# Performance work log

Hardware: AMD Instinct MI355X
Metric: run time of the kernel (lower is better)

## Reference

```python
import jax, jax.numpy as jnp
import numpy as np
import math

B, S, HID = 2, 2048, 2048
NH, HD = 16, HID // 16          # num_heads, head_dim
RING = 4
CH = S // RING                  # chunk size per ring rank
SEG_LEN = 2048                  # segment_lengths[0]
DIL = 2                         # dilation_rates[0]


def setup_inputs() -> dict:
    key = jax.random.key(0)
    k1, k2, k3 = jax.random.split(key, 3)
    x = jax.random.normal(k1, (B, S, HID), dtype=jnp.float32)
    # Linear weights stored input-major so y = x @ W (same math as torch x @ W.T)
    W_qkv = jax.random.normal(k2, (HID, 3 * HID), dtype=jnp.float32) * 0.02
    W_out = jax.random.normal(k3, (HID, HID), dtype=jnp.float32) * 0.02
    return {"x": x, "W_qkv": W_qkv, "W_out": W_out}


def _dilated_mask():
    # mask[i, j] = (segment(i) == segment(j)) and (|i - j| % DIL == 0)
    pos = jnp.arange(S)
    seg = pos // SEG_LEN
    same_seg = seg[:, None] == seg[None, :]
    dil_ok = (jnp.abs(pos[:, None] - pos[None, :]) % DIL) == 0
    return same_seg & dil_ok  # [S, S] bool


def reference(x, W_qkv, W_out):
    qkv = (x @ W_qkv).reshape(B, S, 3, NH, HD)
    q, k, v = jnp.moveaxis(qkv, 2, 0)          # each [B, S, NH, HD]
    q = jnp.transpose(q, (0, 2, 1, 3))          # [B, NH, S, HD]
    k = jnp.transpose(k, (0, 2, 1, 3))
    v = jnp.transpose(v, (0, 2, 1, 3))

    scores = jnp.einsum('bhqd,bhkd->bhqk', q, k) / math.sqrt(HD)  # [B,NH,S,S]
    if DIL > 1:
        scores = jnp.where(_dilated_mask()[None, None], scores, -jnp.inf)

    # Reshape into (q-chunk, kv-chunk) blocks to reproduce the per-chunk
    # (non-rescaled) softmax of the ring loop: each kv chunk subtracts its OWN
    # max, exps, and the un-rescaled numerators/denominators are summed.
    s = scores.reshape(B, NH, RING, CH, RING, CH)        # [B,H,Rq,Cq,Rk,Ck]
    m = jnp.max(s, axis=-1, keepdims=True)               # per-kv-chunk row max
    e = jnp.exp(s - m)                                   # -inf -> 0
    v_ch = v.reshape(B, NH, RING, CH, HD)                # [B,H,Rk,Ck,HD]
    num = jnp.einsum('bhqcrk,bhrkd->bhqcd', e, v_ch)     # [B,H,Rq,Cq,HD]
    den = jnp.sum(e, axis=(-2, -1))[..., None]           # [B,H,Rq,Cq,1]
    out = num / (den + 1e-8)

    out = out.reshape(B, NH, S, HD)
    out = jnp.transpose(out, (0, 2, 1, 3)).reshape(B, S, HID)
    return out @ W_out
```

## Files before the change

kernel.cpp:

```cpp
#include <hip/hip_runtime.h>
#include <stdint.h>

typedef float  f32x4  __attribute__((ext_vector_type(4)));
typedef __bf16 bf16x8 __attribute__((ext_vector_type(8)));

#define AS1 __attribute__((address_space(1)))
#define AS3 __attribute__((address_space(3)))


__global__ void k_cvt_x(const float* __restrict__ x, __bf16* __restrict__ y) {
  const int i = blockIdx.x * 256 + threadIdx.x;
  const float4 v = reinterpret_cast<const float4*>(x)[i];
  union { __bf16 b[4]; uint64_t u; } o;
  o.b[0] = (__bf16)v.x; o.b[1] = (__bf16)v.y; o.b[2] = (__bf16)v.z; o.b[3] = (__bf16)v.w;
  reinterpret_cast<uint64_t*>(y)[i] = o.u;
}

__global__ void k_cvt_wt(const float* __restrict__ w, __bf16* __restrict__ wt,
                         const int K, const int N) {
  __shared__ float tile[64][65];
  const int k0 = blockIdx.x * 64, n0 = blockIdx.y * 64;
  const int t = threadIdx.x;
  #pragma unroll
  for (int i = 0; i < 16; ++i) {
    const int idx = t + 256 * i;
    const int r = idx >> 6, c = idx & 63;
    tile[r][c] = w[(size_t)(k0 + r) * N + n0 + c];
  }
  __syncthreads();
  #pragma unroll
  for (int i = 0; i < 16; ++i) {
    const int idx = t + 256 * i;
    const int r = idx >> 6, c = idx & 63;
    wt[(size_t)(n0 + r) * K + k0 + c] = (__bf16)tile[c][r];
  }
}

template<int EPI>
__global__ __launch_bounds__(256, 2) void k_gemm_bt(
    const __bf16* __restrict__ A, const __bf16* __restrict__ Bt,
    __bf16* __restrict__ Oq, __bf16* __restrict__ Ok, __bf16* __restrict__ Ov,
    float* __restrict__ Of, const int M, const int N, const int K) {
  __shared__ __bf16 As[128 * 32];
  __shared__ __bf16 Bs[128 * 32];
  const int tid = threadIdx.x;
  const int w = tid >> 6, l = tid & 63, g = l >> 4, l15 = l & 15;
  const int wr = w >> 1, wc = w & 1;
  const int m0 = blockIdx.y * 128, n0 = blockIdx.x * 128;
  const int srow = l >> 2, scol = (l & 3) * 8;

  f32x4 acc[4][4] = {};

  for (int kt = 0; kt < K; kt += 32) {
    __syncthreads();
    #pragma unroll
    for (int i = 0; i < 2; ++i) {
      const int ch = w * 2 + i;
      const int row = ch * 16 + srow;
      __builtin_amdgcn_global_load_lds(
          (const AS1 uint32_t*)(A + (size_t)(m0 + row) * K + kt + scol),
          (AS3 uint32_t*)(As + ch * 512), 16, 0, 0);
      __builtin_amdgcn_global_load_lds(
          (const AS1 uint32_t*)(Bt + (size_t)(n0 + row) * K + kt + scol),
          (AS3 uint32_t*)(Bs + ch * 512), 16, 0, 0);
    }
    __syncthreads();

    bf16x8 af[4], bfr[4];
    #pragma unroll
    for (int mi = 0; mi < 4; ++mi)
      af[mi] = *reinterpret_cast<const bf16x8*>(As + (wr * 64 + mi * 16 + l15) * 32 + 8 * g);
    #pragma unroll
    for (int ni = 0; ni < 4; ++ni)
      bfr[ni] = *reinterpret_cast<const bf16x8*>(Bs + (wc * 64 + ni * 16 + l15) * 32 + 8 * g);
    #pragma unroll
    for (int mi = 0; mi < 4; ++mi)
      #pragma unroll
      for (int ni = 0; ni < 4; ++ni)
        acc[mi][ni] = __builtin_amdgcn_mfma_f32_16x16x32_bf16(af[mi], bfr[ni], acc[mi][ni], 0, 0, 0);
  }

  if constexpr (EPI == 1) {
    const int t = n0 >> 11;
    const int h = (n0 & 2047) >> 7;
    const int bb = m0 >> 11;
    #pragma unroll
    for (int mi = 0; mi < 4; ++mi) {
      #pragma unroll
      for (int r = 0; r < 4; ++r) {
        const int m = m0 + wr * 64 + mi * 16 + 4 * g + r;
        const int s = m & 2047;
        const int sp = s & 1, s2 = s >> 1;
        const size_t base = ((((size_t)bb * 16 + h) * 2 + sp) << 17);
        #pragma unroll
        for (int ni = 0; ni < 4; ++ni) {
          const int d = wc * 64 + ni * 16 + l15;
          const __bf16 v = (__bf16)acc[mi][ni][r];
          if (t == 0)      Oq[base + (size_t)s2 * 128 + d] = v;
          else if (t == 1) Ok[base + (size_t)s2 * 128 + d] = v;
          else             Ov[base + (size_t)d * 1024 + s2] = v;
        }
      }
    }
  } else {
    #pragma unroll
    for (int mi = 0; mi < 4; ++mi)
      #pragma unroll
      for (int ni = 0; ni < 4; ++ni)
        #pragma unroll
        for (int r = 0; r < 4; ++r) {
          const int m = m0 + wr * 64 + mi * 16 + 4 * g + r;
          const int n = n0 + wc * 64 + ni * 16 + l15;
          Of[(size_t)m * N + n] = acc[mi][ni][r];
        }
  }
}

__global__ __launch_bounds__(256, 2) void k_attn(
    const __bf16* __restrict__ Qp, const __bf16* __restrict__ Kp,
    const __bf16* __restrict__ Vt, __bf16* __restrict__ attn) {
  __shared__ __bf16 Ks[64 * 128];
  __shared__ __bf16 Vs[128 * 64];
  __shared__ __bf16 E[4][16][136];

  const int bx = blockIdx.x;
  const int wid = (bx & 7) * 128 + (bx >> 3);
  const int qt = wid & 15, p = (wid >> 4) & 1, h = (wid >> 5) & 15, b = wid >> 9;
  const int tid = threadIdx.x;
  const int w = tid >> 6, l = tid & 63, g = l >> 4, l15 = l & 15;
  const size_t base = ((((size_t)b * 16 + h) * 2 + p) << 17);
  const __bf16* Qb = Qp + base;
  const __bf16* Kb = Kp + base;
  const __bf16* Vb = Vt + base;
  const int q0 = qt * 64 + w * 16;
  const float SC = 1.4426950408889634f / 11.313708498984761f;

  bf16x8 qf[4];
  #pragma unroll
  for (int ks = 0; ks < 4; ++ks)
    qf[ks] = *reinterpret_cast<const bf16x8*>(Qb + (size_t)(q0 + l15) * 128 + ks * 32 + 8 * g);

  f32x4 num[8] = {};
  float den[4] = {0.f, 0.f, 0.f, 0.f};

  const int krow_in = l >> 4;
  const int vrow_in = l >> 3;
  const int vsrc_e = (((l & 7) * 16) ^ (vrow_in << 4)) >> 1;

  for (int c = 0; c < 4; ++c) {
    f32x4 s[16] = {};
    #pragma unroll
    for (int st = 0; st < 4; ++st) {
      __syncthreads();
      #pragma unroll
      for (int i = 0; i < 4; ++i) {
        const int ch = w * 4 + i;
        const int row = ch * 4 + krow_in;
        const int cb = (l15 * 16) ^ ((row & 7) << 4);
        const __bf16* src = Kb + (size_t)(c * 256 + st * 64 + row) * 128 + (cb >> 1);
        __builtin_amdgcn_global_load_lds((const AS1 uint32_t*)src,
                                         (AS3 uint32_t*)(Ks + ch * 512), 16, 0, 0);
      }
      __syncthreads();
      #pragma unroll
      for (int ks = 0; ks < 4; ++ks) {
        #pragma unroll
        for (int nf2 = 0; nf2 < 4; ++nf2) {
          const int r = nf2 * 16 + l15;
          const int cb = (ks * 64 + g * 16) ^ ((r & 7) << 4);
          const bf16x8 kf = *reinterpret_cast<const bf16x8*>(Ks + r * 128 + (cb >> 1));
          s[st * 4 + nf2] = __builtin_amdgcn_mfma_f32_16x16x32_bf16(qf[ks], kf, s[st * 4 + nf2], 0, 0, 0);
        }
      }
    }
    float mv[4];
    #pragma unroll
    for (int r = 0; r < 4; ++r) {
      float m0v = s[0][r];
      #pragma unroll
      for (int nf = 1; nf < 16; ++nf) m0v = fmaxf(m0v, s[nf][r]);
      m0v = fmaxf(m0v, __shfl_xor(m0v, 1));
      m0v = fmaxf(m0v, __shfl_xor(m0v, 2));
      m0v = fmaxf(m0v, __shfl_xor(m0v, 4));
      m0v = fmaxf(m0v, __shfl_xor(m0v, 8));
      mv[r] = m0v;
    }
    #pragma unroll
    for (int r = 0; r < 4; ++r) {
      float ds = 0.f;
      #pragma unroll
      for (int nf = 0; nf < 16; ++nf) {
        const float e = exp2f((s[nf][r] - mv[r]) * SC);
        s[nf][r] = e;
        ds += e;
      }
      den[r] += ds;
    }
    #pragma unroll
    for (int h2 = 0; h2 < 2; ++h2) {
      #pragma unroll
      for (int nf = 0; nf < 8; ++nf)
        #pragma unroll
        for (int r = 0; r < 4; ++r)
          E[w][4 * g + r][nf * 16 + l15] = (__bf16)s[h2 * 8 + nf][r];
      #pragma unroll
      for (int sv = 0; sv < 2; ++sv) {
        const int kv0 = c * 256 + h2 * 128 + sv * 64;
        __syncthreads();
        #pragma unroll
        for (int i = 0; i < 4; ++i) {
          const int ch = w * 4 + i;
          const int row = ch * 8 + vrow_in;
          const __bf16* src = Vb + (size_t)row * 1024 + kv0 + vsrc_e;
          __builtin_amdgcn_global_load_lds((const AS1 uint32_t*)src,
                                           (AS3 uint32_t*)(Vs + ch * 512), 16, 0, 0);
        }
        __syncthreads();
        #pragma unroll
        for (int ks2 = 0; ks2 < 2; ++ks2) {
          const bf16x8 a = *reinterpret_cast<const bf16x8*>(
              &E[w][l15][sv * 64 + ks2 * 32 + 8 * g]);
          #pragma unroll
          for (int nd = 0; nd < 8; ++nd) {
            const int d = nd * 16 + l15;
            const int cb = (ks2 * 64 + g * 16) ^ ((d & 7) << 4);
            const bf16x8 vf = *reinterpret_cast<const bf16x8*>(Vs + d * 64 + (cb >> 1));
            num[nd] = __builtin_amdgcn_mfma_f32_16x16x32_bf16(a, vf, num[nd], 0, 0, 0);
          }
        }
      }
    }
  }

  #pragma unroll
  for (int r = 0; r < 4; ++r) {
    den[r] += __shfl_xor(den[r], 1);
    den[r] += __shfl_xor(den[r], 2);
    den[r] += __shfl_xor(den[r], 4);
    den[r] += __shfl_xor(den[r], 8);
    den[r] += 1e-8f;
  }

  #pragma unroll
  for (int nd = 0; nd < 8; ++nd)
    #pragma unroll
    for (int r = 0; r < 4; ++r) {
      const int sq = q0 + 4 * g + r;
      const int srow = 2 * sq + p;
      attn[((size_t)b * 2048 + srow) * 2048 + h * 128 + nd * 16 + l15] =
          (__bf16)(num[nd][r] / den[r]);
    }
}

extern "C" void kernel_launch(void* const* d_in, const int* in_sizes, int n_in,
                              void* d_out, int out_size, void* d_ws, size_t ws_size,
                              hipStream_t stream) {
  (void)in_sizes; (void)n_in; (void)out_size; (void)ws_size;
  const float* x    = (const float*)d_in[0];
  const float* wqkv = (const float*)d_in[1];
  const float* wout = (const float*)d_in[2];
  float* out = (float*)d_out;
  uint8_t* ws = (uint8_t*)d_ws;

  __bf16* xbf   = (__bf16*)(ws + 0);
  __bf16* wqkvt = (__bf16*)(ws + (16ull << 20));
  __bf16* woutt = (__bf16*)(ws + (40ull << 20));
  __bf16* Qp    = (__bf16*)(ws + (48ull << 20));
  __bf16* Kp    = (__bf16*)(ws + (64ull << 20));
  __bf16* Vt    = (__bf16*)(ws + (80ull << 20));
  __bf16* attn  = (__bf16*)(ws + 0);

  k_cvt_x<<<8192, 256, 0, stream>>>(x, xbf);
  k_cvt_wt<<<dim3(32, 96), 256, 0, stream>>>(wqkv, wqkvt, 2048, 6144);
  k_cvt_wt<<<dim3(32, 32), 256, 0, stream>>>(wout, woutt, 2048, 2048);
  k_gemm_bt<1><<<dim3(48, 32), 256, 0, stream>>>(xbf, wqkvt, Qp, Kp, Vt, nullptr, 4096, 6144, 2048);
  k_attn<<<1024, 256, 0, stream>>>(Qp, Kp, Vt, attn);
  k_gemm_bt<2><<<dim3(16, 32), 256, 0, stream>>>(attn, woutt, nullptr, nullptr, nullptr, out, 4096, 2048, 2048);
}
```

Before: 297.0 us.

## Pre-block QKV GEMM operands and triple-buffer its K loop

The x and W_qkv conversion kernels now write bf16 data in a tile-blocked layout that matches the LDS tile order, so each GEMM stage is a contiguous copy. The QKV GEMM is replaced by a new kernel that triple-buffers LDS with global_load_lds prefetch two tiles ahead, uses one barrier per step with vmcnt waits, and raises MFMA priority. It also remaps block IDs across XCDs. The aim is to hide global load latency and cut sync overhead in the largest GEMM, at the cost of more LDS per block (occupancy target raised to 3) and more complex conversion indexing.

```diff
diff --git a/kernel.cpp b/kernel.cpp
--- a/kernel.cpp
+++ b/kernel.cpp
@@ -8,12 +8,17 @@
 #define AS3 __attribute__((address_space(3)))
 
 
-__global__ void k_cvt_x(const float* __restrict__ x, __bf16* __restrict__ y) {
-  const int i = blockIdx.x * 256 + threadIdx.x;
-  const float4 v = reinterpret_cast<const float4*>(x)[i];
-  union { __bf16 b[4]; uint64_t u; } o;
-  o.b[0] = (__bf16)v.x; o.b[1] = (__bf16)v.y; o.b[2] = (__bf16)v.z; o.b[3] = (__bf16)v.w;
-  reinterpret_cast<uint64_t*>(y)[i] = o.u;
+__global__ void k_cvt_x_blk(const float* __restrict__ x, __bf16* __restrict__ y) {
+  const int d = blockIdx.x * 256 + threadIdx.x;
+  const int row = d & 127, kg = (d >> 7) & 3, mbkt = d >> 9;
+  const int mb = mbkt & 31, kt = mbkt >> 5;
+  const int m = mb * 128 + row, k0 = kt * 32 + kg * 8;
+  const float4 v0 = *reinterpret_cast<const float4*>(x + (size_t)m * 2048 + k0);
+  const float4 v1 = *reinterpret_cast<const float4*>(x + (size_t)m * 2048 + k0 + 4);
+  bf16x8 o;
+  o[0] = (__bf16)v0.x; o[1] = (__bf16)v0.y; o[2] = (__bf16)v0.z; o[3] = (__bf16)v0.w;
+  o[4] = (__bf16)v1.x; o[5] = (__bf16)v1.y; o[6] = (__bf16)v1.z; o[7] = (__bf16)v1.w;
+  *reinterpret_cast<bf16x8*>(y + (size_t)d * 8) = o;
 }
 
 __global__ void k_cvt_wt(const float* __restrict__ w, __bf16* __restrict__ wt,
@@ -36,10 +41,115 @@
   }
 }
 
-template<int EPI>
-__global__ __launch_bounds__(256, 2) void k_gemm_bt(
+__global__ void k_cvt_wt_blk(const float* __restrict__ w, __bf16* __restrict__ wt,
+                             const int N, const int NBK) {
+  __shared__ float tile[64][65];
+  const int k0 = blockIdx.x * 64, n0 = blockIdx.y * 64;
+  const int t = threadIdx.x;
+  #pragma unroll
+  for (int i = 0; i < 16; ++i) {
+    const int idx = t + 256 * i;
+    const int r = idx >> 6, c = idx & 63;
+    tile[r][c] = w[(size_t)(k0 + r) * N + n0 + c];
+  }
+  __syncthreads();
+  #pragma unroll
+  for (int i = 0; i < 16; ++i) {
+    const int idx = t + 256 * i;
+    const int nn = idx >> 6, kk = idx & 63;
+    const int n = n0 + nn, k = k0 + kk;
+    const size_t dst = ((size_t)(k >> 5) * NBK + (n >> 7)) * 4096 +
+                       (size_t)((k >> 3) & 3) * 1024 + (n & 127) * 8 + (k & 7);
+    wt[dst] = (__bf16)tile[kk][nn];
+  }
+}
+
+__global__ __launch_bounds__(256, 3) void k_gemm1p(
+    const __bf16* __restrict__ Ab, const __bf16* __restrict__ Bb,
+    __bf16* __restrict__ Oq, __bf16* __restrict__ Ok, __bf16* __restrict__ Ov) {
+  __shared__ __bf16 As[3][4096];
+  __shared__ __bf16 Bs[3][4096];
+  const int tid = threadIdx.x;
+  const int w = tid >> 6, l = tid & 63, g = l >> 4, l15 = l & 15;
+  const int wr = w >> 1, wc = w & 1;
+  const int bx = blockIdx.x;
+  const int wid = (bx & 7) * 192 + (bx >> 3);
+  const int nb = wid % 48, mb = wid / 48;
+  const size_t Abase = (size_t)mb * 4096, Bbase = (size_t)nb * 4096;
+  const size_t Astep = 32 * 4096, Bstep = 48 * 4096;
+  const int soff = w * 1024;
+
+  f32x4 acc[4][4] = {};
+
+  auto STAGE = [&](int t, int b) {
+    const __bf16* as_ = Ab + (size_t)t * Astep + Abase + soff + l * 8;
+    const __bf16* bs_ = Bb + (size_t)t * Bstep + Bbase + soff + l * 8;
+    __builtin_amdgcn_global_load_lds((const AS1 uint32_t*)as_,
+                                     (AS3 uint32_t*)(&As[b][soff]), 16, 0, 0);
+    __builtin_amdgcn_global_load_lds((const AS1 uint32_t*)(as_ + 512),
+                                     (AS3 uint32_t*)(&As[b][soff + 512]), 16, 0, 0);
+    __builtin_amdgcn_global_load_lds((const AS1 uint32_t*)bs_,
+                                     (AS3 uint32_t*)(&Bs[b][soff]), 16, 0, 0);
+    __builtin_amdgcn_global_load_lds((const AS1 uint32_t*)(bs_ + 512),
+                                     (AS3 uint32_t*)(&Bs[b][soff + 512]), 16, 0, 0);
+  };
+
+  STAGE(0, 0);
+  STAGE(1, 1);
+  asm volatile("s_waitcnt vmcnt(4)" ::: "memory");
+  __builtin_amdgcn_s_barrier();
+
+  int cur = 0;
+  for (int t = 0; t < 64; ++t) {
+    int b2 = cur + 2; if (b2 >= 3) b2 -= 3;
+    if (t + 2 < 64) STAGE(t + 2, b2);
+    const __bf16* Ar = &As[cur][g * 1024 + (wr * 64 + l15) * 8];
+    const __bf16* Br = &Bs[cur][g * 1024 + (wc * 64 + l15) * 8];
+    bf16x8 af[4], bfr[4];
+    #pragma unroll
+    for (int mi = 0; mi < 4; ++mi) af[mi] = *reinterpret_cast<const bf16x8*>(Ar + mi * 128);
+    #pragma unroll
+    for (int ni = 0; ni < 4; ++ni) bfr[ni] = *reinterpret_cast<const bf16x8*>(Br + ni * 128);
+    __builtin_amdgcn_s_setprio(1);
+    #pragma unroll
+    for (int mi = 0; mi < 4; ++mi)
+      #pragma unroll
+      for (int ni = 0; ni < 4; ++ni)
+        acc[mi][ni] = __builtin_amdgcn_mfma_f32_16x16x32_bf16(af[mi], bfr[ni], acc[mi][ni], 0, 0, 0);
+    __builtin_amdgcn_s_setprio(0);
+    __builtin_amdgcn_sched_barrier(0);
+    if (t < 62) asm volatile("s_waitcnt vmcnt(4)" ::: "memory");
+    else        asm volatile("s_waitcnt vmcnt(0)" ::: "memory");
+    __builtin_amdgcn_s_barrier();
+    cur = cur + 1; if (cur >= 3) cur -= 3;
+  }
+
+  const int m0 = mb * 128, n0 = nb * 128;
+  const int ty = n0 >> 11;
+  const int h = (n0 & 2047) >> 7;
+  #pragma unroll
+  for (int mi = 0; mi < 4; ++mi) {
+    #pragma unroll
+    for (int r = 0; r < 4; ++r) {
+      const int m = m0 + wr * 64 + mi * 16 + 4 * g + r;
+      const int s = m & 2047;
+      const int sp = s & 1, s2 = s >> 1;
+      const int bb = m >> 11;
+      const size_t base = ((((size_t)bb * 16 + h) * 2 + sp) << 17);
+      #pragma unroll
+      for (int ni = 0; ni < 4; ++ni) {
+        const int d = wc * 64 + ni * 16 + l15;
+        const __bf16 v = (__bf16)acc[mi][ni][r];
+        if (ty == 0)      Oq[base + (size_t)s2 * 128 + d] = v;
+        else if (ty == 1) Ok[base + (size_t)s2 * 128 + d] = v;
+        else              Ov[base + (size_t)d * 1024 + s2] = v;
+      }
+    }
+  }
+}
+
+__global__ __launch_bounds__(256, 2) void k_gemm_bt2(
     const __bf16* __restrict__ A, const __bf16* __restrict__ Bt,
-    __bf16* __restrict__ Oq, __bf16* __restrict__ Ok, __bf16* __restrict__ Ov,
     float* __restrict__ Of, const int M, const int N, const int K) {
   __shared__ __bf16 As[128 * 32];
   __shared__ __bf16 Bs[128 * 32];
@@ -80,40 +190,16 @@
         acc[mi][ni] = __builtin_amdgcn_mfma_f32_16x16x32_bf16(af[mi], bfr[ni], acc[mi][ni], 0, 0, 0);
   }
 
-  if constexpr (EPI == 1) {
-    const int t = n0 >> 11;
-    const int h = (n0 & 2047) >> 7;
-    const int bb = m0 >> 11;
-    #pragma unroll
-    for (int mi = 0; mi < 4; ++mi) {
+  #pragma unroll
+  for (int mi = 0; mi < 4; ++mi)
+    #pragma unroll
+    for (int ni = 0; ni < 4; ++ni)
       #pragma unroll
       for (int r = 0; r < 4; ++r) {
         const int m = m0 + wr * 64 + mi * 16 + 4 * g + r;
-        const int s = m & 2047;
-        const int sp = s & 1, s2 = s >> 1;
-        const size_t base = ((((size_t)bb * 16 + h) * 2 + sp) << 17);
-        #pragma unroll
-        for (int ni = 0; ni < 4; ++ni) {
-          const int d = wc * 64 + ni * 16 + l15;
-          const __bf16 v = (__bf16)acc[mi][ni][r];
-          if (t == 0)      Oq[base + (size_t)s2 * 128 + d] = v;
-          else if (t == 1) Ok[base + (size_t)s2 * 128 + d] = v;
-          else             Ov[base + (size_t)d * 1024 + s2] = v;
-        }
-      }
-    }
-  } else {
-    #pragma unroll
-    for (int mi = 0; mi < 4; ++mi)
-      #pragma unroll
-      for (int ni = 0; ni < 4; ++ni)
-        #pragma unroll
-        for (int r = 0; r < 4; ++r) {
-          const int m = m0 + wr * 64 + mi * 16 + 4 * g + r;
-          const int n = n0 + wc * 64 + ni * 16 + l15;
-          Of[(size_t)m * N + n] = acc[mi][ni][r];
-        }
-  }
+        const int n = n0 + wc * 64 + ni * 16 + l15;
+        Of[(size_t)m * N + n] = acc[mi][ni][r];
+      }
 }
 
 __global__ __launch_bounds__(256, 2) void k_attn(
@@ -270,10 +356,10 @@
   __bf16* Vt    = (__bf16*)(ws + (80ull << 20));
   __bf16* attn  = (__bf16*)(ws + 0);
 
-  k_cvt_x<<<8192, 256, 0, stream>>>(x, xbf);
-  k_cvt_wt<<<dim3(32, 96), 256, 0, stream>>>(wqkv, wqkvt, 2048, 6144);
+  k_cvt_x_blk<<<4096, 256, 0, stream>>>(x, xbf);
+  k_cvt_wt_blk<<<dim3(32, 96), 256, 0, stream>>>(wqkv, wqkvt, 6144, 48);
   k_cvt_wt<<<dim3(32, 32), 256, 0, stream>>>(wout, woutt, 2048, 2048);
-  k_gemm_bt<1><<<dim3(48, 32), 256, 0, stream>>>(xbf, wqkvt, Qp, Kp, Vt, nullptr, 4096, 6144, 2048);
+  k_gemm1p<<<1536, 256, 0, stream>>>(xbf, wqkvt, Qp, Kp, Vt);
   k_attn<<<1024, 256, 0, stream>>>(Qp, Kp, Vt, attn);
-  k_gemm_bt<2><<<dim3(16, 32), 256, 0, stream>>>(attn, woutt, nullptr, nullptr, nullptr, out, 4096, 2048, 2048);
-}
+  k_gemm_bt2<<<dim3(16, 32), 256, 0, stream>>>(attn, woutt, out, 4096, 2048, 2048);
+}
```

Result: faster. 285.8 us (-3.8%).
